# Optimization experiments

Hardware: AMD Instinct MI355X
Metric: run time of the kernel (lower is better)

Reference implementation:

```python
import jax, jax.numpy as jnp
import numpy as np

VOCAB, EMB, H, LAYERS, B, T = 50000, 128, 128, 3, 64, 512


def _lstm_dir(x, w_ih, w_hh, b_ih, b_hh, h0, c0, reverse):
    # x: [B,T,Din]; w_ih: [4H,Din]; w_hh: [4H,H]; h0,c0: [B,H]
    xg = jnp.einsum('btd,gd->btg', x, w_ih) + b_ih + b_hh  # [B,T,4H]

    def step(carry, xg_t):
        h, c = carry
        g = xg_t + h @ w_hh.T  # [B,4H]
        i, f, gg, o = jnp.split(g, 4, axis=-1)  # torch gate order i,f,g,o
        c = jax.nn.sigmoid(f) * c + jax.nn.sigmoid(i) * jnp.tanh(gg)
        h = jax.nn.sigmoid(o) * jnp.tanh(c)
        return (h, c), h

    _, hs = jax.lax.scan(step, (h0, c0), jnp.swapaxes(xg, 0, 1), reverse=reverse)
    return jnp.swapaxes(hs, 0, 1)  # [B,T,H], aligned with input time order


def _bidir_layer(x, w_ih, w_hh, b_ih, b_hh, h0, c0):
    # stacked params: leading dim 2 = (fwd, bwd)
    fwd = _lstm_dir(x, w_ih[0], w_hh[0], b_ih[0], b_hh[0], h0[0], c0[0], False)
    bwd = _lstm_dir(x, w_ih[1], w_hh[1], b_ih[1], b_hh[1], h0[1], c0[1], True)
    return jnp.concatenate([fwd, bwd], axis=-1)  # [B,T,2H]


def setup_inputs() -> dict:
    key = jax.random.key(0)
    ks = jax.random.split(key, 20)
    s = 1.0 / np.sqrt(H)
    inp = {
        'X_batch': jax.random.randint(ks[0], (B, T), 0, VOCAB),
        'emb': jax.random.normal(ks[1], (VOCAB, EMB), jnp.float32),
        'hx': jax.random.normal(ks[2], (2 * LAYERS, B, H), jnp.float32),
        'cx': jax.random.normal(ks[3], (2 * LAYERS, B, H), jnp.float32),
        'lin_w': jax.random.uniform(ks[4], (1, 2 * H), jnp.float32, -s, s),
        'lin_b': jax.random.uniform(ks[5], (1,), jnp.float32, -s, s),
    }
    k = 6
    for l in range(LAYERS):
        din = EMB if l == 0 else 2 * H
        inp[f'w_ih_{l}'] = jax.random.uniform(ks[k], (2, 4 * H, din), jnp.float32, -s, s); k += 1
        inp[f'w_hh_{l}'] = jax.random.uniform(ks[k], (2, 4 * H, H), jnp.float32, -s, s); k += 1
        inp[f'b_ih_{l}'] = jax.random.uniform(ks[k], (2, 4 * H), jnp.float32, -s, s); k += 1
        inp[f'b_hh_{l}'] = jax.random.uniform(ks[k], (2, 4 * H), jnp.float32, -s, s); k += 1
    return inp


def reference(X_batch, emb, hx, cx, lin_w, lin_b,
              w_ih_0, w_hh_0, b_ih_0, b_hh_0,
              w_ih_1, w_hh_1, b_ih_1, b_hh_1,
              w_ih_2, w_hh_2, b_ih_2, b_hh_2):
    x = emb[X_batch]  # [B,T,EMB]
    params = [(w_ih_0, w_hh_0, b_ih_0, b_hh_0),
              (w_ih_1, w_hh_1, b_ih_1, b_hh_1),
              (w_ih_2, w_hh_2, b_ih_2, b_hh_2)]
    for l, (wi, wh, bi, bh) in enumerate(params):
        x = _bidir_layer(x, wi, wh, bi, bh, hx[2 * l:2 * l + 2], cx[2 * l:2 * l + 2])
    # linear head applied to last timestep (== output[:, -1] of full linear)
    return x[:, -1] @ lin_w.T + lin_b  # [B,1]
```

## Files before the change

### kernel.cpp

```cpp
#include <hip/hip_runtime.h>
#include <hip/hip_bf16.h>
#include <stdint.h>

#define B_    64
#define T_    512
#define EMB_  128
#define H_    128
#define G4    512
#define M_    (B_ * T_)

typedef __attribute__((ext_vector_type(8))) short     short8;
typedef __attribute__((ext_vector_type(4))) float     floatx4;
typedef __attribute__((ext_vector_type(2))) _Float16  half2v;

#define GLDS(g, l) __builtin_amdgcn_global_load_lds( \
    (__attribute__((address_space(1))) void*)(g),    \
    (__attribute__((address_space(3))) void*)(l), 16, 0, 0)

__device__ __forceinline__ unsigned short f2bf_bits(float f) {
  __hip_bfloat16 h = __float2bfloat16(f);
  return *reinterpret_cast<unsigned short*>(&h);
}
__device__ __forceinline__ float bf_bits2f(unsigned short u) {
  unsigned int x = ((unsigned int)u) << 16;
  return __uint_as_float(x);
}
__device__ __forceinline__ float sigm(float x) {
  return __fdividef(1.0f, 1.0f + __expf(-x));
}
__device__ __forceinline__ float tanh_fast(float x) {
  return 1.0f - __fdividef(2.0f, __expf(2.0f * x) + 1.0f);
}

__device__ __forceinline__ unsigned int pack_f16x2(float a, float b) {
  half2v h; h.x = (_Float16)a; h.y = (_Float16)b;
  return __builtin_bit_cast(unsigned int, h);
}
__device__ __forceinline__ half2v u2h2(unsigned int u) {
  return __builtin_bit_cast(half2v, u);
}

#if __has_builtin(__builtin_amdgcn_fdot2)
__device__ __forceinline__ float fdot2(half2v a, half2v b, float c) {
  return __builtin_amdgcn_fdot2(a, b, c, false);
}
#else
__device__ __forceinline__ float fdot2(half2v a, half2v b, float c) {
  return fmaf((float)a.x, (float)b.x, fmaf((float)a.y, (float)b.y, c));
}
#endif

__device__ __forceinline__ float quad_bfly_add(float x) {
  float y = x + __int_as_float(
      __builtin_amdgcn_mov_dpp(__float_as_int(x), 0xB1, 0xF, 0xF, true));
  return y + __int_as_float(
      __builtin_amdgcn_mov_dpp(__float_as_int(y), 0x4E, 0xF, 0xF, true));
}

__device__ __forceinline__ void barrier_lds_only() {
  __builtin_amdgcn_s_waitcnt(0xC07F);
  __builtin_amdgcn_s_barrier();
}

__device__ __forceinline__ void  store_xg(float* p, float v)  { *p = v; }
__device__ __forceinline__ void  store_xg(unsigned short* p, float v) { *p = f2bf_bits(v); }
__device__ __forceinline__ float load_xg(const float* p)  { return *p; }
__device__ __forceinline__ float load_xg(const unsigned short* p) { return bf_bits2f(*p); }

__global__ void k_gather(const int* __restrict__ X, const float* __restrict__ emb,
                         unsigned short* __restrict__ x0) {
  int i = blockIdx.x * 256 + threadIdx.x;
  int row = i >> 5, c4 = i & 31;
  float4 v = ((const float4*)emb)[(size_t)X[row] * 32 + c4];
  ushort4 o;
  o.x = f2bf_bits(v.x); o.y = f2bf_bits(v.y); o.z = f2bf_bits(v.z); o.w = f2bf_bits(v.w);
  ((ushort4*)x0)[i] = o;
}

__global__ void k_prep(const float* __restrict__ w, const float* __restrict__ bi,
                       const float* __restrict__ bh, unsigned short* __restrict__ wb,
                       float* __restrict__ bias, int nw) {
  int i = blockIdx.x * blockDim.x + threadIdx.x;
  int stride = gridDim.x * blockDim.x;
  for (int k = i; k < nw; k += stride) wb[k] = f2bf_bits(w[k]);
  for (int k = i; k < 2 * G4; k += stride) bias[k] = bi[k] + bh[k];
}

__global__ void k_prep_whh(const float* __restrict__ Whh, unsigned int* __restrict__ wf) {
  int i = blockIdx.x * 256 + threadIdx.x;
  int dir = i >> 15;
  int t2  = i & 0x7FFF;
  int jq  = t2 >> 11;
  int t3  = t2 & 0x7FF;
  int ts  = t3 >> 2;
  int q   = t3 & 3;
  int d   = jq * 4 + q;
  int g   = d >> 4;
  int jj  = d & 15;
  int lane = ts & 63, wave = ts >> 6;
  int p = lane & 3, ul = lane >> 2;
  int u = wave * 16 + ul;
  int k = 32 * p + 2 * jj;
  const float* wr = Whh + ((size_t)dir * G4 + g * H_ + u) * H_ + k;
  wf[i] = pack_f16x2(wr[0], wr[1]);
}

template <typename XG_T>
__global__ __launch_bounds__(256, 2) void k_gemm(
    const unsigned short* __restrict__ A,
    const unsigned short* __restrict__ W,
    const float* __restrict__ bias,
    XG_T* __restrict__ xg,
    int K) {
  __shared__ unsigned short sA[128 * 32];
  __shared__ unsigned short sB[128 * 32];
  const int tid  = threadIdx.x;
  const int lane = tid & 63;
  const int wave = tid >> 6;
  const int mt = blockIdx.x, nt = blockIdx.y, dir = blockIdx.z;
  const size_t Arow0 = (size_t)mt * 128;
  const int    Ncol0 = nt * 128;
  const unsigned short* Wd = W + (size_t)dir * G4 * K;

  const int srow = tid >> 2;
  const int qlog = (tid & 3) ^ ((tid >> 4) & 3);
  auto ldsA0 = (__attribute__((address_space(3))) void*)(sA + wave * 512);
  auto ldsA1 = (__attribute__((address_space(3))) void*)(sA + 2048 + wave * 512);
  auto ldsB0 = (__attribute__((address_space(3))) void*)(sB + wave * 512);
  auto ldsB1 = (__attribute__((address_space(3))) void*)(sB + 2048 + wave * 512);

  floatx4 acc[4][4];
#pragma unroll
  for (int i = 0; i < 4; ++i)
#pragma unroll
    for (int j = 0; j < 4; ++j) acc[i][j] = (floatx4)0.0f;

  const int wrow = (wave >> 1) * 64, wcol = (wave & 1) * 64;
  const int frow = lane & 15;
  const int fq   = lane >> 4;

  for (int kt = 0; kt < K; kt += 32) {
    const unsigned short* gA0 = A  + (Arow0 + srow) * (size_t)K + kt + qlog * 8;
    const unsigned short* gB0 = Wd + (size_t)(Ncol0 + srow) * K + kt + qlog * 8;
    GLDS(gA0, ldsA0);
    GLDS(gA0 + (size_t)64 * K, ldsA1);
    GLDS(gB0, ldsB0);
    GLDS(gB0 + (size_t)64 * K, ldsB1);
    __syncthreads();

    short8 af[4], bf[4];
#pragma unroll
    for (int i = 0; i < 4; ++i) {
      int r  = wrow + 16 * i + frow;
      int rn = wcol + 16 * i + frow;
      af[i] = *(const short8*)(sA + r  * 32 + ((fq ^ ((r  >> 2) & 3)) * 8));
      bf[i] = *(const short8*)(sB + rn * 32 + ((fq ^ ((rn >> 2) & 3)) * 8));
    }
#pragma unroll
    for (int i = 0; i < 4; ++i)
#pragma unroll
      for (int j = 0; j < 4; ++j)
        acc[i][j] = __builtin_amdgcn_mfma_f32_16x16x32_bf16(af[i], bf[j], acc[i][j], 0, 0, 0);
    __syncthreads();
  }

  const int r0 = (lane >> 4) * 4;
  const int cc = lane & 15;
  XG_T* xgd = xg + (size_t)dir * M_ * G4;
#pragma unroll
  for (int j = 0; j < 4; ++j) {
    int gcol = Ncol0 + wcol + 16 * j + cc;
    float bs = bias[dir * G4 + gcol];
#pragma unroll
    for (int i = 0; i < 4; ++i) {
      size_t rowb = Arow0 + wrow + 16 * i + r0;
#pragma unroll
      for (int r = 0; r < 4; ++r)
        store_xg(&xgd[(rowb + r) * G4 + gcol], acc[i][j][r] + bs);
    }
  }
}

template <typename XG_T>
__global__ __attribute__((amdgpu_flat_work_group_size(512, 512),
                          amdgpu_waves_per_eu(2, 2))) void k_scan(
    const unsigned int* __restrict__ wf,
    const float* __restrict__ hx0,
    const float* __restrict__ cx0,
    const XG_T* __restrict__ xg,
    unsigned short* __restrict__ y)
{
  const int b   = blockIdx.x & 63;
  const int dir = blockIdx.x >> 6;
  const int tid = threadIdx.x;
  const int lane = tid & 63;
  const int wave = tid >> 6;
  const int p  = lane & 3;
  const int ul = lane >> 2;
  const int u  = wave * 16 + ul;

  __shared__ __align__(16) unsigned short h16[2][128];

  uint4 wv[16];
  const uint4* wfv = (const uint4*)wf;
#pragma unroll
  for (int i = 0; i < 16; ++i) wv[i] = wfv[(dir * 16 + i) * 512 + tid];

  float c = cx0[(size_t)dir * B_ * H_ + b * H_ + u];
  if (p == 0) {
    float h0 = hx0[(size_t)dir * B_ * H_ + b * H_ + u];
    h16[0][u] = (unsigned short)(pack_f16x2(h0, 0.0f) & 0xFFFF);
  }

  const XG_T* xgb = xg + ((size_t)dir * M_ + (size_t)b * T_) * G4;
  const intptr_t xstep = dir ? -(intptr_t)G4 : (intptr_t)G4;
  const XG_T* xrow0 = xgb + (dir ? (size_t)(T_ - 1) * G4 : 0) + p * H_ + u;
  float xp0 = load_xg(xrow0);
  float xp1 = load_xg(xrow0 + xstep);
  const XG_T* xld = xrow0 + 2 * xstep;

  unsigned short* yp = y + ((size_t)b * T_ + (dir ? T_ - 1 : 0)) * (2 * H_)
                         + dir * H_ + u;
  const intptr_t ystep = dir ? -(intptr_t)(2 * H_) : (intptr_t)(2 * H_);

  __syncthreads();

  auto dots = [&](int par, float xv, float& g0, float& g1, float& g2, float& g3) {
    const uint4* hv4 = (const uint4*)&h16[par][0];
    uint4 h0v = hv4[4 * p + 0], h1v = hv4[4 * p + 1];
    uint4 h2v = hv4[4 * p + 2], h3v = hv4[4 * p + 3];
    half2v hh[16] = {
      u2h2(h0v.x), u2h2(h0v.y), u2h2(h0v.z), u2h2(h0v.w),
      u2h2(h1v.x), u2h2(h1v.y), u2h2(h1v.z), u2h2(h1v.w),
      u2h2(h2v.x), u2h2(h2v.y), u2h2(h2v.z), u2h2(h2v.w),
      u2h2(h3v.x), u2h2(h3v.y), u2h2(h3v.z), u2h2(h3v.w)};
    float a0 = 0, b0 = 0, a1 = 0, b1 = 0, a2 = 0, b2 = 0, a3 = 0, b3 = 0;
#pragma unroll
    for (int j = 0; j < 8; ++j) {
      a0 = fdot2(u2h2(((const unsigned int*)&wv[(0 * 16 + j) >> 2])[(0 * 16 + j) & 3]), hh[j], a0);
      a1 = fdot2(u2h2(((const unsigned int*)&wv[(1 * 16 + j) >> 2])[(1 * 16 + j) & 3]), hh[j], a1);
      a2 = fdot2(u2h2(((const unsigned int*)&wv[(2 * 16 + j) >> 2])[(2 * 16 + j) & 3]), hh[j], a2);
      a3 = fdot2(u2h2(((const unsigned int*)&wv[(3 * 16 + j) >> 2])[(3 * 16 + j) & 3]), hh[j], a3);
      int j8 = j + 8;
      b0 = fdot2(u2h2(((const unsigned int*)&wv[(0 * 16 + j8) >> 2])[(0 * 16 + j8) & 3]), hh[j8], b0);
      b1 = fdot2(u2h2(((const unsigned int*)&wv[(1 * 16 + j8) >> 2])[(1 * 16 + j8) & 3]), hh[j8], b1);
      b2 = fdot2(u2h2(((const unsigned int*)&wv[(2 * 16 + j8) >> 2])[(2 * 16 + j8) & 3]), hh[j8], b2);
      b3 = fdot2(u2h2(((const unsigned int*)&wv[(3 * 16 + j8) >> 2])[(3 * 16 + j8) & 3]), hh[j8], b3);
    }
    g0 = a0 + b0; g1 = a1 + b1; g2 = a2 + b2; g3 = a3 + b3;
    g0 += (p == 0) ? xv : 0.0f;
    g1 += (p == 1) ? xv : 0.0f;
    g2 += (p == 2) ? xv : 0.0f;
    g3 += (p == 3) ? xv : 0.0f;
  };

  auto finish = [&](int par, float g0, float g1, float g2, float g3) {
    g0 = quad_bfly_add(g0);
    g1 = quad_bfly_add(g1);
    g2 = quad_bfly_add(g2);
    g3 = quad_bfly_add(g3);
    float iv = sigm(g0), fv = sigm(g1), gv = tanh_fast(g2), ov = sigm(g3);
    c = fmaf(fv, c, iv * gv);
    float h = ov * tanh_fast(c);
    if (p == 0) {
      h16[par ^ 1][u] = (unsigned short)(pack_f16x2(h, 0.0f) & 0xFFFF);
      *yp = f2bf_bits(h);
    }
    yp += ystep;
    barrier_lds_only();
  };

  for (int t = 0; t < T_; t += 2) {
    float a0, a1, a2, a3;
    dots(0, xp0, a0, a1, a2, a3);
    xp0 = (t + 2 < T_) ? load_xg(xld) : 0.0f;
    xld += xstep;
    finish(0, a0, a1, a2, a3);
    dots(1, xp1, a0, a1, a2, a3);
    xp1 = (t + 3 < T_) ? load_xg(xld) : 0.0f;
    xld += xstep;
    finish(1, a0, a1, a2, a3);
  }
}

__global__ void k_head(const unsigned short* __restrict__ y2, const float* __restrict__ lw,
                       const float* __restrict__ lb, float* __restrict__ out) {
  int b = blockIdx.x, l = threadIdx.x;
  const unsigned short* row = y2 + ((size_t)b * T_ + (T_ - 1)) * (2 * H_);
  float s = 0;
#pragma unroll
  for (int k = 0; k < 4; ++k) s += bf_bits2f(row[l + 64 * k]) * lw[l + 64 * k];
#pragma unroll
  for (int off = 32; off > 0; off >>= 1) s += __shfl_down(s, off);
  if (l == 0) out[b] = s + lb[0];
}

template <typename XG_T>
static inline void run_layers(const unsigned int* const* wfs,
                              const unsigned short* x0,
                              unsigned short* y0, unsigned short* y1, unsigned short* y2,
                              const unsigned short* wb0, const unsigned short* wb1,
                              const unsigned short* wb2,
                              const float* bias0, const float* bias1, const float* bias2,
                              const float* hx, const float* cx,
                              XG_T* xg, hipStream_t stream) {
  dim3 gg(M_ / 128, G4 / 128, 2);
  k_gemm<XG_T><<<gg, 256, 0, stream>>>(x0, wb0, bias0, xg, EMB_);
  k_scan<XG_T><<<128, 512, 0, stream>>>(wfs[0], hx, cx, xg, y0);
  k_gemm<XG_T><<<gg, 256, 0, stream>>>(y0, wb1, bias1, xg, 2 * H_);
  k_scan<XG_T><<<128, 512, 0, stream>>>(wfs[1], hx + 2 * B_ * H_, cx + 2 * B_ * H_, xg, y1);
  k_gemm<XG_T><<<gg, 256, 0, stream>>>(y1, wb2, bias2, xg, 2 * H_);
  k_scan<XG_T><<<128, 512, 0, stream>>>(wfs[2], hx + 4 * B_ * H_, cx + 4 * B_ * H_, xg, y2);
}

extern "C" void kernel_launch(void* const* d_in, const int* in_sizes, int n_in,
                              void* d_out, int out_size, void* d_ws, size_t ws_size,
                              hipStream_t stream) {
  const int*   X   = (const int*)d_in[0];
  const float* emb = (const float*)d_in[1];
  const float* hx  = (const float*)d_in[2];
  const float* cx  = (const float*)d_in[3];
  const float* lw  = (const float*)d_in[4];
  const float* lb  = (const float*)d_in[5];
  const float* w_ih[3] = {(const float*)d_in[6],  (const float*)d_in[10], (const float*)d_in[14]};
  const float* w_hh[3] = {(const float*)d_in[7],  (const float*)d_in[11], (const float*)d_in[15]};
  const float* b_ih[3] = {(const float*)d_in[8],  (const float*)d_in[12], (const float*)d_in[16]};
  const float* b_hh[3] = {(const float*)d_in[9],  (const float*)d_in[13], (const float*)d_in[17]};
  float* out = (float*)d_out;

  char* ws = (char*)d_ws;
  size_t off = 0;
  auto carve = [&](size_t bytes) {
    char* p = ws + off;
    off = (off + bytes + 255) & ~(size_t)255;
    return p;
  };
  unsigned short* x0  = (unsigned short*)carve((size_t)M_ * EMB_ * 2);
  unsigned short* y0  = (unsigned short*)carve((size_t)M_ * 2 * H_ * 2);
  unsigned short* y1  = (unsigned short*)carve((size_t)M_ * 2 * H_ * 2);
  unsigned short* y2  = (unsigned short*)carve((size_t)M_ * 2 * H_ * 2);
  unsigned short* wb0 = (unsigned short*)carve((size_t)2 * G4 * EMB_ * 2);
  unsigned short* wb1 = (unsigned short*)carve((size_t)2 * G4 * 2 * H_ * 2);
  unsigned short* wb2 = (unsigned short*)carve((size_t)2 * G4 * 2 * H_ * 2);
  float* bias0 = (float*)carve(2 * G4 * 4);
  float* bias1 = (float*)carve(2 * G4 * 4);
  float* bias2 = (float*)carve(2 * G4 * 4);
  unsigned int* wf0 = (unsigned int*)carve((size_t)65536 * 4);
  unsigned int* wf1 = (unsigned int*)carve((size_t)65536 * 4);
  unsigned int* wf2 = (unsigned int*)carve((size_t)65536 * 4);
  const size_t xg_f32_bytes = (size_t)2 * M_ * G4 * 4;
  const bool use_f32 = (off + xg_f32_bytes) <= ws_size;
  void* xg = carve(use_f32 ? xg_f32_bytes : xg_f32_bytes / 2);

  k_prep<<<256, 256, 0, stream>>>(w_ih[0], b_ih[0], b_hh[0], wb0, bias0, 2 * G4 * EMB_);
  k_prep<<<256, 256, 0, stream>>>(w_ih[1], b_ih[1], b_hh[1], wb1, bias1, 2 * G4 * 2 * H_);
  k_prep<<<256, 256, 0, stream>>>(w_ih[2], b_ih[2], b_hh[2], wb2, bias2, 2 * G4 * 2 * H_);
  k_prep_whh<<<256, 256, 0, stream>>>(w_hh[0], wf0);
  k_prep_whh<<<256, 256, 0, stream>>>(w_hh[1], wf1);
  k_prep_whh<<<256, 256, 0, stream>>>(w_hh[2], wf2);
  k_gather<<<(M_ * 32) / 256, 256, 0, stream>>>(X, emb, x0);

  const unsigned int* wfs[3] = {wf0, wf1, wf2};
  if (use_f32)
    run_layers<float>(wfs, x0, y0, y1, y2, wb0, wb1, wb2, bias0, bias1, bias2,
                      hx, cx, (float*)xg, stream);
  else
    run_layers<unsigned short>(wfs, x0, y0, y1, y2, wb0, wb1, wb2, bias0, bias1, bias2,
                               hx, cx, (unsigned short*)xg, stream);

  k_head<<<64, 64, 0, stream>>>(y2, lw, lb, out);
}
```

Measured before the change: 1.375 ms.

## Stage gate inputs into LDS per chunk and batch hidden-state writes

```diff
diff --git a/kernel.cpp b/kernel.cpp
--- a/kernel.cpp
+++ b/kernel.cpp
@@ -8,6 +8,7 @@
 #define H_    128
 #define G4    512
 #define M_    (B_ * T_)
+#define CH    8
 
 typedef __attribute__((ext_vector_type(8))) short     short8;
 typedef __attribute__((ext_vector_type(4))) float     floatx4;
@@ -171,12 +172,13 @@
   for (int j = 0; j < 4; ++j) {
     int gcol = Ncol0 + wcol + 16 * j + cc;
     float bs = bias[dir * G4 + gcol];
+    int pcol = 4 * (gcol & 127) + (gcol >> 7);
 #pragma unroll
     for (int i = 0; i < 4; ++i) {
       size_t rowb = Arow0 + wrow + 16 * i + r0;
 #pragma unroll
       for (int r = 0; r < 4; ++r)
-        store_xg(&xgd[(rowb + r) * G4 + gcol], acc[i][j][r] + bs);
+        store_xg(&xgd[(rowb + r) * G4 + pcol], acc[i][j][r] + bs);
     }
   }
 }
@@ -200,6 +202,8 @@
   const int u  = wave * 16 + ul;
 
   __shared__ __align__(16) unsigned short h16[2][128];
+  __shared__ __align__(16) XG_T           xbuf[2][CH * G4];
+  __shared__ __align__(16) unsigned short ybuf[2][CH * H_];
 
   uint4 wv[16];
   const uint4* wfv = (const uint4*)wf;
@@ -213,73 +217,93 @@
   }
 
   const XG_T* xgb = xg + ((size_t)dir * M_ + (size_t)b * T_) * G4;
-  const intptr_t xstep = dir ? -(intptr_t)G4 : (intptr_t)G4;
-  const XG_T* xrow0 = xgb + (dir ? (size_t)(T_ - 1) * G4 : 0) + p * H_ + u;
-  float xp0 = load_xg(xrow0);
-  float xp1 = load_xg(xrow0 + xstep);
-  const XG_T* xld = xrow0 + 2 * xstep;
-
-  unsigned short* yp = y + ((size_t)b * T_ + (dir ? T_ - 1 : 0)) * (2 * H_)
-                         + dir * H_ + u;
-  const intptr_t ystep = dir ? -(intptr_t)(2 * H_) : (intptr_t)(2 * H_);
-
+
+  auto stage = [&](int cidx) {
+    const int nIss = (CH * G4 * (int)sizeof(XG_T)) / 8192;
+#pragma unroll
+    for (int i = 0; i < nIss; ++i) {
+      int ebyte = i * 8192 + tid * 16;
+      int e   = ebyte / (int)sizeof(XG_T);
+      int r   = e >> 9;
+      int win = e & 511;
+      int tt  = dir ? (T_ - 1 - (cidx * CH + r)) : (cidx * CH + r);
+      const XG_T* src = xgb + (size_t)tt * G4 + win;
+      auto dst = (__attribute__((address_space(3))) void*)
+          ((char*)&xbuf[cidx & 1][0] + i * 8192 + wave * 1024);
+      GLDS(src, dst);
+    }
+  };
+
+  auto flush = [&](int cidx) {
+    int s  = tid >> 6;
+    int up = tid & 63;
+    unsigned int v = ((const unsigned int*)&ybuf[cidx & 1][0])[tid];
+    int tt = dir ? (T_ - 1 - (cidx * CH + s)) : (cidx * CH + s);
+    ((unsigned int*)y)[(((size_t)b * T_ + tt) * (2 * H_) + dir * H_) / 2 + up] = v;
+  };
+
+  stage(0);
   __syncthreads();
-
-  auto dots = [&](int par, float xv, float& g0, float& g1, float& g2, float& g3) {
-    const uint4* hv4 = (const uint4*)&h16[par][0];
-    uint4 h0v = hv4[4 * p + 0], h1v = hv4[4 * p + 1];
-    uint4 h2v = hv4[4 * p + 2], h3v = hv4[4 * p + 3];
-    half2v hh[16] = {
-      u2h2(h0v.x), u2h2(h0v.y), u2h2(h0v.z), u2h2(h0v.w),
-      u2h2(h1v.x), u2h2(h1v.y), u2h2(h1v.z), u2h2(h1v.w),
-      u2h2(h2v.x), u2h2(h2v.y), u2h2(h2v.z), u2h2(h2v.w),
-      u2h2(h3v.x), u2h2(h3v.y), u2h2(h3v.z), u2h2(h3v.w)};
-    float a0 = 0, b0 = 0, a1 = 0, b1 = 0, a2 = 0, b2 = 0, a3 = 0, b3 = 0;
-#pragma unroll
-    for (int j = 0; j < 8; ++j) {
-      a0 = fdot2(u2h2(((const unsigned int*)&wv[(0 * 16 + j) >> 2])[(0 * 16 + j) & 3]), hh[j], a0);
-      a1 = fdot2(u2h2(((const unsigned int*)&wv[(1 * 16 + j) >> 2])[(1 * 16 + j) & 3]), hh[j], a1);
-      a2 = fdot2(u2h2(((const unsigned int*)&wv[(2 * 16 + j) >> 2])[(2 * 16 + j) & 3]), hh[j], a2);
-      a3 = fdot2(u2h2(((const unsigned int*)&wv[(3 * 16 + j) >> 2])[(3 * 16 + j) & 3]), hh[j], a3);
-      int j8 = j + 8;
-      b0 = fdot2(u2h2(((const unsigned int*)&wv[(0 * 16 + j8) >> 2])[(0 * 16 + j8) & 3]), hh[j8], b0);
-      b1 = fdot2(u2h2(((const unsigned int*)&wv[(1 * 16 + j8) >> 2])[(1 * 16 + j8) & 3]), hh[j8], b1);
-      b2 = fdot2(u2h2(((const unsigned int*)&wv[(2 * 16 + j8) >> 2])[(2 * 16 + j8) & 3]), hh[j8], b2);
-      b3 = fdot2(u2h2(((const unsigned int*)&wv[(3 * 16 + j8) >> 2])[(3 * 16 + j8) & 3]), hh[j8], b3);
-    }
-    g0 = a0 + b0; g1 = a1 + b1; g2 = a2 + b2; g3 = a3 + b3;
-    g0 += (p == 0) ? xv : 0.0f;
-    g1 += (p == 1) ? xv : 0.0f;
-    g2 += (p == 2) ? xv : 0.0f;
-    g3 += (p == 3) ? xv : 0.0f;
-  };
-
-  auto finish = [&](int par, float g0, float g1, float g2, float g3) {
-    g0 = quad_bfly_add(g0);
-    g1 = quad_bfly_add(g1);
-    g2 = quad_bfly_add(g2);
-    g3 = quad_bfly_add(g3);
-    float iv = sigm(g0), fv = sigm(g1), gv = tanh_fast(g2), ov = sigm(g3);
-    c = fmaf(fv, c, iv * gv);
-    float h = ov * tanh_fast(c);
-    if (p == 0) {
-      h16[par ^ 1][u] = (unsigned short)(pack_f16x2(h, 0.0f) & 0xFFFF);
-      *yp = f2bf_bits(h);
-    }
-    yp += ystep;
-    barrier_lds_only();
-  };
-
-  for (int t = 0; t < T_; t += 2) {
-    float a0, a1, a2, a3;
-    dots(0, xp0, a0, a1, a2, a3);
-    xp0 = (t + 2 < T_) ? load_xg(xld) : 0.0f;
-    xld += xstep;
-    finish(0, a0, a1, a2, a3);
-    dots(1, xp1, a0, a1, a2, a3);
-    xp1 = (t + 3 < T_) ? load_xg(xld) : 0.0f;
-    xld += xstep;
-    finish(1, a0, a1, a2, a3);
+  stage(1);
+
+  const int NCH = T_ / CH;
+  for (int cidx = 0; cidx < NCH; ++cidx) {
+    const int buf = cidx & 1;
+#pragma unroll
+    for (int s = 0; s < CH; ++s) {
+      const int gstep = cidx * CH + s;
+      const int par = gstep & 1;
+      float xv = load_xg(&xbuf[buf][s * G4 + wave * 64 + lane]);
+
+      const uint4* hv4 = (const uint4*)&h16[par][0];
+      uint4 h0v = hv4[4 * p + 0], h1v = hv4[4 * p + 1];
+      uint4 h2v = hv4[4 * p + 2], h3v = hv4[4 * p + 3];
+      half2v hh[16] = {
+        u2h2(h0v.x), u2h2(h0v.y), u2h2(h0v.z), u2h2(h0v.w),
+        u2h2(h1v.x), u2h2(h1v.y), u2h2(h1v.z), u2h2(h1v.w),
+        u2h2(h2v.x), u2h2(h2v.y), u2h2(h2v.z), u2h2(h2v.w),
+        u2h2(h3v.x), u2h2(h3v.y), u2h2(h3v.z), u2h2(h3v.w)};
+      float a0 = 0, b0 = 0, a1 = 0, b1 = 0, a2 = 0, b2 = 0, a3 = 0, b3 = 0;
+#pragma unroll
+      for (int j = 0; j < 8; ++j) {
+        a0 = fdot2(u2h2(((const unsigned int*)&wv[(0 * 16 + j) >> 2])[(0 * 16 + j) & 3]), hh[j], a0);
+        a1 = fdot2(u2h2(((const unsigned int*)&wv[(1 * 16 + j) >> 2])[(1 * 16 + j) & 3]), hh[j], a1);
+        a2 = fdot2(u2h2(((const unsigned int*)&wv[(2 * 16 + j) >> 2])[(2 * 16 + j) & 3]), hh[j], a2);
+        a3 = fdot2(u2h2(((const unsigned int*)&wv[(3 * 16 + j) >> 2])[(3 * 16 + j) & 3]), hh[j], a3);
+        int j8 = j + 8;
+        b0 = fdot2(u2h2(((const unsigned int*)&wv[(0 * 16 + j8) >> 2])[(0 * 16 + j8) & 3]), hh[j8], b0);
+        b1 = fdot2(u2h2(((const unsigned int*)&wv[(1 * 16 + j8) >> 2])[(1 * 16 + j8) & 3]), hh[j8], b1);
+        b2 = fdot2(u2h2(((const unsigned int*)&wv[(2 * 16 + j8) >> 2])[(2 * 16 + j8) & 3]), hh[j8], b2);
+        b3 = fdot2(u2h2(((const unsigned int*)&wv[(3 * 16 + j8) >> 2])[(3 * 16 + j8) & 3]), hh[j8], b3);
+      }
+      float g0 = a0 + b0, g1 = a1 + b1, g2 = a2 + b2, g3 = a3 + b3;
+      g0 += (p == 0) ? xv : 0.0f;
+      g1 += (p == 1) ? xv : 0.0f;
+      g2 += (p == 2) ? xv : 0.0f;
+      g3 += (p == 3) ? xv : 0.0f;
+
+      g0 = quad_bfly_add(g0);
+      g1 = quad_bfly_add(g1);
+      g2 = quad_bfly_add(g2);
+      g3 = quad_bfly_add(g3);
+
+      float iv = sigm(g0), fv = sigm(g1), gv = tanh_fast(g2), ov = sigm(g3);
+      c = fmaf(fv, c, iv * gv);
+      float h = ov * tanh_fast(c);
+
+      if (p == 0) {
+        h16[par ^ 1][u] = (unsigned short)(pack_f16x2(h, 0.0f) & 0xFFFF);
+        ybuf[buf][s * H_ + u] = f2bf_bits(h);
+      }
+      barrier_lds_only();
+    }
+    if (cidx + 1 < NCH) {
+      __syncthreads();
+      flush(cidx);
+      if (cidx + 2 < NCH) stage(cidx + 2);
+    } else {
+      flush(cidx);
+    }
   }
 }
 
```

Measured after the change: 1.666 ms. 1.21x slower.
